# Performance work log

Measured on AMD Instinct MI355X. Metric: run time of the kernel, lower is better.

## Reference

```python
import jax, jax.numpy as jnp
import numpy as np
import math

D, H, FF, B, S = 512, 8, 2048, 2, 2048
DK = D // H


def _ln(x, g, b, eps=1e-5):
    m = jnp.mean(x, axis=-1, keepdims=True)
    v = jnp.var(x, axis=-1, keepdims=True)
    return (x - m) / jnp.sqrt(v + eps) * g + b


def _mha(q_in, kv_in, Wq, bq, Wk, bk, Wv, bv, Wo, bo):
    Bq, Sq, _ = q_in.shape
    Sk = kv_in.shape[1]
    q = (q_in @ Wq + bq).reshape(Bq, Sq, H, DK).transpose(0, 2, 1, 3)
    k = (kv_in @ Wk + bk).reshape(Bq, Sk, H, DK).transpose(0, 2, 1, 3)
    v = (kv_in @ Wv + bv).reshape(Bq, Sk, H, DK).transpose(0, 2, 1, 3)
    # NOTE: source uses float floor-division `//` by sqrt(dk); replicate faithfully.
    scores = jnp.floor(jnp.einsum('bhqd,bhkd->bhqk', q, k) / math.sqrt(DK))
    # NOTE: source calls scores.masked_fill(...) without assigning -> mask has no effect.
    attn = jax.nn.softmax(scores, axis=-1)
    out = jnp.einsum('bhqk,bhkd->bhqd', attn, v)
    out = out.transpose(0, 2, 1, 3).reshape(Bq, Sq, D)
    return out @ Wo + bo


def setup_inputs() -> dict:
    key = jax.random.key(0)
    ks = jax.random.split(key, 16)
    w = lambda k, shp: jax.random.normal(k, shp, jnp.float32) * 0.02
    inp = {
        'x': jax.random.normal(ks[0], (B, S, D), jnp.float32),
        'enc_out': jax.random.normal(ks[1], (B, S, D), jnp.float32),
        'src_mask': jnp.ones((B, 1, 1, S), jnp.int32),
        'tgt_mask': jnp.ones((B, 1, S, S), jnp.int32),
    }
    for i, pre in enumerate(['sa', 'ca']):
        kk = jax.random.split(ks[2 + i], 4)
        for j, nm in enumerate(['Wq', 'Wk', 'Wv', 'Wo']):
            inp[f'{pre}_{nm}'] = w(kk[j], (D, D))
            inp[f'{pre}_{nm[1].lower()}b'] = jnp.zeros((D,), jnp.float32)
    inp['ff_W1'] = w(ks[4], (D, FF)); inp['ff_b1'] = jnp.zeros((FF,), jnp.float32)
    inp['ff_W2'] = w(ks[5], (FF, D)); inp['ff_b2'] = jnp.zeros((D,), jnp.float32)
    for i in range(3):
        inp[f'ln{i}_g'] = jnp.ones((D,), jnp.float32)
        inp[f'ln{i}_b'] = jnp.zeros((D,), jnp.float32)
    return inp


def reference(x, enc_out, src_mask, tgt_mask,
              sa_Wq, sa_qb, sa_Wk, sa_kb, sa_Wv, sa_vb, sa_Wo, sa_ob,
              ca_Wq, ca_qb, ca_Wk, ca_kb, ca_Wv, ca_vb, ca_Wo, ca_ob,
              ff_W1, ff_b1, ff_W2, ff_b2,
              ln0_g, ln0_b, ln1_g, ln1_b, ln2_g, ln2_b):
    x = _ln(x + _mha(x, x, sa_Wq, sa_qb, sa_Wk, sa_kb, sa_Wv, sa_vb, sa_Wo, sa_ob), ln0_g, ln0_b)
    x = _ln(x + _mha(x, enc_out, ca_Wq, ca_qb, ca_Wk, ca_kb, ca_Wv, ca_vb, ca_Wo, ca_ob), ln1_g, ln1_b)
    ff = jax.nn.relu(x @ ff_W1 + ff_b1) @ ff_W2 + ff_b2
    x = _ln(x + ff, ln2_g, ln2_b)
    return x
```

## Files before the change

### kernel.cpp

```cpp
#include <hip/hip_runtime.h>
#include <math.h>


typedef __attribute__((ext_vector_type(8))) short short8;
typedef __attribute__((ext_vector_type(4))) float f32x4;

#define MFMA16(a, b, c) __builtin_amdgcn_mfma_f32_16x16x32_bf16((a), (b), (c), 0, 0, 0)

__device__ __forceinline__ unsigned short f2bf(float f) {
    unsigned int u = __float_as_uint(f);
    u += 0x7fffu + ((u >> 16) & 1u);
    return (unsigned short)(u >> 16);
}
__device__ __forceinline__ float bf2f(unsigned short h) {
    return __uint_as_float(((unsigned int)h) << 16);
}
__device__ __forceinline__ void g2l16(const void* g, void* l) {
    __builtin_amdgcn_global_load_lds(
        (const __attribute__((address_space(1))) unsigned int*)g,
        (__attribute__((address_space(3))) unsigned int*)l, 16, 0, 0);
}
__device__ __forceinline__ int swz(int row, int col) {
    return row * 64 + (col ^ ((row & 7) * 8));
}
__device__ __forceinline__ void xcd_remap(int& bx, int& by, int& bz) {
    const int gx = gridDim.x, gy = gridDim.y;
    const int nwg = gx * gy * gridDim.z;
    const int flat = blockIdx.x + gx * (blockIdx.y + gy * blockIdx.z);
    const int s = (flat & 7) * (nwg >> 3) + (flat >> 3);
    bx = s % gx; const int t = s / gx; by = t % gy; bz = t / gy;
}

template <int BM, int BN, int MODE>
__global__ __launch_bounds__(256, (BM == 64) ? 4 : (BN == 128 ? 2 : 3))
void gemm_bf16(
    const unsigned short* __restrict__ A, const unsigned short* __restrict__ Bt,
    const float* __restrict__ bias, float* __restrict__ Cf,
    unsigned short* __restrict__ O1,
    int M, int N, int K)
{
    __shared__ unsigned short As[2][BM * 64];
    __shared__ unsigned short Bs[2][BN * 64];
    const int tid = threadIdx.x, wv = tid >> 6, lane = tid & 63;
    const int l15 = lane & 15, l4 = lane >> 4;
    int bx, by, bz; xcd_remap(bx, by, bz);
    const int bm = by * BM, bn = bx * BN;
    constexpr int MI = (BM == 64) ? 1 : (BN == 128 ? 4 : 2);
    constexpr int AJ = (BM == 64) ? 2 : 4;
    constexpr int BJ = (BN == 128) ? 4 : 2;
    const int wrow = (BM == 64) ? wv * 16 : (BN == 128 ? (wv >> 1) * 64 : wv * 32);
    const int wcol = (BN == 128) ? (wv & 1) * 64 : 0;
    const int aw = (BM == 64) ? wv * 16 : wv * 32;
    const int bw = (BN == 128) ? wv * 32 : wv * 16;

    f32x4 acc[MI][4];
    #pragma unroll
    for (int i = 0; i < MI; ++i)
        #pragma unroll
        for (int j = 0; j < 4; ++j) acc[i][j] = (f32x4){0.f, 0.f, 0.f, 0.f};

    const int srow = lane >> 3;
    const int sch  = (lane & 7) ^ srow;
    const unsigned short* Asrc = A + (size_t)(bm + aw + srow) * K + sch * 8;
    const unsigned short* Bsrc = Bt + (size_t)(bn + bw + srow) * K + sch * 8;

    auto stage = [&](int buf, int k0) {
        #pragma unroll
        for (int j = 0; j < AJ; ++j)
            g2l16(Asrc + (size_t)j * 8 * K + k0, &As[buf][(aw + j * 8) * 64]);
        #pragma unroll
        for (int j = 0; j < BJ; ++j)
            g2l16(Bsrc + (size_t)j * 8 * K + k0, &Bs[buf][(bw + j * 8) * 64]);
    };

    stage(0, 0);
    __syncthreads();
    int cur = 0;
    for (int k0 = 0; k0 < K; k0 += 64) {
        if (k0 + 64 < K) stage(cur ^ 1, k0 + 64);
        #pragma unroll
        for (int kk = 0; kk < 2; ++kk) {
            const int kc = kk * 32 + l4 * 8;
            short8 af[MI], bfr[4];
            #pragma unroll
            for (int mi = 0; mi < MI; ++mi)
                af[mi] = *(const short8*)&As[cur][swz(wrow + mi * 16 + l15, kc)];
            #pragma unroll
            for (int nf = 0; nf < 4; ++nf)
                bfr[nf] = *(const short8*)&Bs[cur][swz(wcol + nf * 16 + l15, kc)];
            __builtin_amdgcn_s_setprio(1);
            #pragma unroll
            for (int mi = 0; mi < MI; ++mi)
                #pragma unroll
                for (int nf = 0; nf < 4; ++nf)
                    acc[mi][nf] = MFMA16(af[mi], bfr[nf], acc[mi][nf]);
            __builtin_amdgcn_s_setprio(0);
        }
        __syncthreads();
        cur ^= 1;
    }

    #pragma unroll
    for (int nf = 0; nf < 4; ++nf) {
        const int n = bn + wcol + nf * 16 + l15;
        const float bv = bias[n];
        #pragma unroll
        for (int mi = 0; mi < MI; ++mi) {
            const int m0 = bm + wrow + mi * 16 + l4 * 4;
            #pragma unroll
            for (int r = 0; r < 4; ++r) {
                float v = acc[mi][nf][r] + bv;
                size_t idx = (size_t)(m0 + r) * N + n;
                if (MODE == 0)      Cf[idx] = v;
                else if (MODE == 3) O1[idx] = f2bf(fmaxf(v, 0.f));
                else                O1[idx] = f2bf(v);
            }
        }
    }
}

struct QKVArgs {
    const unsigned short* A[3];
    const unsigned short* Bt[3];
    const float* bias[3];
    unsigned short* O1[3];
    int mode[3];
};
__global__ __launch_bounds__(256, 3) void qkv_gemm(QKVArgs ja)
{
    __shared__ unsigned short As[2][128 * 64];
    __shared__ unsigned short Bs[2][64 * 64];
    const int tid = threadIdx.x, wv = tid >> 6, lane = tid & 63;
    const int l15 = lane & 15, l4 = lane >> 4;
    int bx, by, bz; xcd_remap(bx, by, bz);
    const int bm = by * 128, bn = bx * 64;
    const unsigned short* A  = ja.A[bz];
    const unsigned short* Bt = ja.Bt[bz];
    const int mode = ja.mode[bz];

    f32x4 acc[2][4];
    #pragma unroll
    for (int i = 0; i < 2; ++i)
        #pragma unroll
        for (int j = 0; j < 4; ++j) acc[i][j] = (f32x4){0.f, 0.f, 0.f, 0.f};

    const int srow = lane >> 3, sch = (lane & 7) ^ srow;
    const unsigned short* Asrc = A + (size_t)(bm + wv * 32 + srow) * 512 + sch * 8;
    const unsigned short* Bsrc = Bt + (size_t)(bn + wv * 16 + srow) * 512 + sch * 8;

    auto stage = [&](int buf, int k0) {
        #pragma unroll
        for (int j = 0; j < 4; ++j)
            g2l16(Asrc + (size_t)j * 8 * 512 + k0, &As[buf][(wv * 32 + j * 8) * 64]);
        #pragma unroll
        for (int j = 0; j < 2; ++j)
            g2l16(Bsrc + (size_t)j * 8 * 512 + k0, &Bs[buf][(wv * 16 + j * 8) * 64]);
    };

    stage(0, 0);
    __syncthreads();
    int cur = 0;
    for (int k0 = 0; k0 < 512; k0 += 64) {
        if (k0 + 64 < 512) stage(cur ^ 1, k0 + 64);
        #pragma unroll
        for (int kk = 0; kk < 2; ++kk) {
            const int kc = kk * 32 + l4 * 8;
            short8 af[2], bfr[4];
            af[0] = *(const short8*)&As[cur][swz(wv * 32 + l15, kc)];
            af[1] = *(const short8*)&As[cur][swz(wv * 32 + 16 + l15, kc)];
            #pragma unroll
            for (int nf = 0; nf < 4; ++nf)
                bfr[nf] = *(const short8*)&Bs[cur][swz(nf * 16 + l15, kc)];
            __builtin_amdgcn_s_setprio(1);
            #pragma unroll
            for (int mi = 0; mi < 2; ++mi)
                #pragma unroll
                for (int nf = 0; nf < 4; ++nf)
                    acc[mi][nf] = MFMA16(af[mi], bfr[nf], acc[mi][nf]);
            __builtin_amdgcn_s_setprio(0);
        }
        __syncthreads();
        cur ^= 1;
    }

    #pragma unroll
    for (int nf = 0; nf < 4; ++nf) {
        const int n = bn + nf * 16 + l15;
        const float bv = ja.bias[bz][n];
        #pragma unroll
        for (int mi = 0; mi < 2; ++mi) {
            const int m0 = bm + wv * 32 + mi * 16 + l4 * 4;
            if (mode == 2) {
                const int hh = n >> 6, dd = n & 63, bb = m0 >> 11;
                const int key = m0 & 2047;
                const int f = (key & 63) >> 4, j0 = key & 15;
                const size_t basevt = (((size_t)bb * 8 + hh) * 64 + dd) * 2048
                                    + (key & ~63) + f;
                #pragma unroll
                for (int r = 0; r < 4; ++r)
                    ja.O1[bz][basevt + (size_t)(j0 + r) * 4] = f2bf(acc[mi][nf][r] + bv);
            } else {
                #pragma unroll
                for (int r = 0; r < 4; ++r)
                    ja.O1[bz][(size_t)(m0 + r) * 512 + n] = f2bf(acc[mi][nf][r] + bv);
            }
        }
    }
}

__global__ __launch_bounds__(256, 2) void attn_mfma(
    const unsigned short* __restrict__ Qb, const unsigned short* __restrict__ Kb,
    const unsigned short* __restrict__ Vt,
    float* __restrict__ PO0, float* __restrict__ PO1, float* __restrict__ PL)
{
    __shared__ unsigned short KH[2][64 * 64];
    __shared__ unsigned short VT[2][64 * 64];
    __shared__ unsigned short PS[64 * 64];

    const int tid = threadIdx.x, wv = tid >> 6, lane = tid & 63;
    const int l15 = lane & 15, l4 = lane >> 4;
    int bx, by, bz; xcd_remap(bx, by, bz);
    const int bh = by, b = bh >> 3, h = bh & 7;
    const int q0 = bx * 64;
    const int srow = lane >> 3;
    const int sch  = (lane & 7) ^ srow;
    const int kt0 = bz * 16, kt1 = kt0 + 16;

    short8 qh[2];
    {
        const size_t qrow = (size_t)(b * 2048 + q0 + wv * 16 + l15) * 512 + h * 64;
        qh[0] = *(const short8*)(Qb + qrow + l4 * 8);
        qh[1] = *(const short8*)(Qb + qrow + 32 + l4 * 8);
    }

    const unsigned short* k_src  = Kb + (size_t)(b * 2048 + wv * 16 + srow) * 512 + h * 64 + sch * 8;
    const unsigned short* vt_src = Vt + (size_t)(bh * 64 + wv * 16 + srow) * 2048 + sch * 8;

    auto stageKV = [&](int buf, int kt) {
        const size_t k0 = (size_t)kt * 64;
        #pragma unroll
        for (int j = 0; j < 2; ++j) {
            g2l16(k_src + (k0 + j * 8) * 512, &KH[buf][(wv * 16 + j * 8) * 64]);
            g2l16(vt_src + k0 + (size_t)j * 8 * 2048, &VT[buf][(wv * 16 + j * 8) * 64]);
        }
    };

    f32x4 o[4], lacc;
    #pragma unroll
    for (int i = 0; i < 4; ++i) o[i] = (f32x4){0.f, 0.f, 0.f, 0.f};
    lacc = (f32x4){0.f, 0.f, 0.f, 0.f};

    const short one_s = (short)(l15 == 0 ? 0x3F80 : 0);
    const short8 oneb = {one_s, one_s, one_s, one_s, one_s, one_s, one_s, one_s};

    stageKV(0, kt0);
    __syncthreads();
    int cur = 0;
    for (int kt = kt0; kt < kt1; ++kt) {
        if (kt + 1 < kt1) stageKV(cur ^ 1, kt + 1);

        f32x4 s[4];
        __builtin_amdgcn_s_setprio(1);
        #pragma unroll
        for (int f = 0; f < 4; ++f) {
            s[f] = (f32x4){0.f, 0.f, 0.f, 0.f};
            #pragma unroll
            for (int kk = 0; kk < 2; ++kk) {
                short8 kbf = *(const short8*)&KH[cur][swz(f * 16 + l15, kk * 32 + l4 * 8)];
                s[f] = MFMA16(qh[kk], kbf, s[f]);
            }
        }
        __builtin_amdgcn_s_setprio(0);

        #pragma unroll
        for (int r = 0; r < 4; ++r) {
            float p0 = __expf(floorf(s[0][r] * 0.125f));
            float p1 = __expf(floorf(s[1][r] * 0.125f));
            float p2 = __expf(floorf(s[2][r] * 0.125f));
            float p3 = __expf(floorf(s[3][r] * 0.125f));
            unsigned u0, u1;
            asm("v_cvt_pk_bf16_f32 %0, %1, %2" : "=v"(u0) : "v"(p0), "v"(p1));
            asm("v_cvt_pk_bf16_f32 %0, %1, %2" : "=v"(u1) : "v"(p2), "v"(p3));
            *(uint2*)&PS[swz(wv * 16 + l4 * 4 + r, l15 * 4)] = (uint2){u0, u1};
        }

        short8 pa[2];
        pa[0] = *(const short8*)&PS[swz(wv * 16 + l15, l4 * 8)];
        pa[1] = *(const short8*)&PS[swz(wv * 16 + l15, 32 + l4 * 8)];

        __builtin_amdgcn_s_setprio(1);
        lacc = MFMA16(pa[0], oneb, lacc);
        lacc = MFMA16(pa[1], oneb, lacc);
        #pragma unroll
        for (int df = 0; df < 4; ++df) {
            #pragma unroll
            for (int kk = 0; kk < 2; ++kk) {
                short8 vb = *(const short8*)&VT[cur][swz(df * 16 + l15, kk * 32 + l4 * 8)];
                o[df] = MFMA16(pa[kk], vb, o[df]);
            }
        }
        __builtin_amdgcn_s_setprio(0);
        __syncthreads();
        cur ^= 1;
    }

    float* PO = bz ? PO1 : PO0;
    #pragma unroll
    for (int df = 0; df < 4; ++df)
        #pragma unroll
        for (int r = 0; r < 4; ++r)
            PO[(size_t)(b * 2048 + q0 + wv * 16 + l4 * 4 + r) * 512 + h * 64 + df * 16 + l15]
                = o[df][r];
    if (l15 == 0) {
        #pragma unroll
        for (int r = 0; r < 4; ++r)
            PL[(bz * 16 + bh) * 2048 + q0 + wv * 16 + l4 * 4 + r] = lacc[r];
    }
}

__global__ __launch_bounds__(256) void attn_combine(
    const float* __restrict__ po0, const float* __restrict__ po1,
    const float* __restrict__ pl, unsigned short* __restrict__ Ob)
{
    const size_t i = ((size_t)blockIdx.x * 256 + threadIdx.x) * 8;
    const int row = (int)(i >> 9), col = (int)(i & 511);
    const int b = row >> 11, q = row & 2047, h = col >> 6;
    const int bh = b * 8 + h;
    const float inv = 1.f / (pl[bh * 2048 + q] + pl[(16 + bh) * 2048 + q]);
    float4 a0 = *(const float4*)(po0 + i), a1 = *(const float4*)(po0 + i + 4);
    float4 c0 = *(const float4*)(po1 + i), c1 = *(const float4*)(po1 + i + 4);
    uint4 u;
    u.x = (unsigned)f2bf((a0.x + c0.x) * inv) | ((unsigned)f2bf((a0.y + c0.y) * inv) << 16);
    u.y = (unsigned)f2bf((a0.z + c0.z) * inv) | ((unsigned)f2bf((a0.w + c0.w) * inv) << 16);
    u.z = (unsigned)f2bf((a1.x + c1.x) * inv) | ((unsigned)f2bf((a1.y + c1.y) * inv) << 16);
    u.w = (unsigned)f2bf((a1.z + c1.z) * inv) | ((unsigned)f2bf((a1.w + c1.w) * inv) << 16);
    *(uint4*)(Ob + i) = u;
}

template <bool XBF, bool RBF, bool OUTF, bool OUTB>
__global__ __launch_bounds__(256) void add_ln(
    const void* __restrict__ Xv, const void* __restrict__ Rv,
    const float* __restrict__ g, const float* __restrict__ beta,
    float* __restrict__ OutF, unsigned short* __restrict__ OutB)
{
    const int row = blockIdx.x * 4 + (threadIdx.x >> 6);
    const int lane = threadIdx.x & 63;
    const int c0 = lane * 8;
    float xx[8], rr[8], v[8];
    if (XBF) {
        const unsigned short* xr = (const unsigned short*)Xv + (size_t)row * 512 + c0;
        uint4 u = *(const uint4*)xr;
        xx[0] = bf2f(u.x & 0xffff); xx[1] = bf2f(u.x >> 16);
        xx[2] = bf2f(u.y & 0xffff); xx[3] = bf2f(u.y >> 16);
        xx[4] = bf2f(u.z & 0xffff); xx[5] = bf2f(u.z >> 16);
        xx[6] = bf2f(u.w & 0xffff); xx[7] = bf2f(u.w >> 16);
    } else {
        const float* xr = (const float*)Xv + (size_t)row * 512 + c0;
        float4 a0 = *(const float4*)xr, a1 = *(const float4*)(xr + 4);
        xx[0] = a0.x; xx[1] = a0.y; xx[2] = a0.z; xx[3] = a0.w;
        xx[4] = a1.x; xx[5] = a1.y; xx[6] = a1.z; xx[7] = a1.w;
    }
    if (RBF) {
        const unsigned short* xr = (const unsigned short*)Rv + (size_t)row * 512 + c0;
        uint4 u = *(const uint4*)xr;
        rr[0] = bf2f(u.x & 0xffff); rr[1] = bf2f(u.x >> 16);
        rr[2] = bf2f(u.y & 0xffff); rr[3] = bf2f(u.y >> 16);
        rr[4] = bf2f(u.z & 0xffff); rr[5] = bf2f(u.z >> 16);
        rr[6] = bf2f(u.w & 0xffff); rr[7] = bf2f(u.w >> 16);
    } else {
        const float* xr = (const float*)Rv + (size_t)row * 512 + c0;
        float4 a0 = *(const float4*)xr, a1 = *(const float4*)(xr + 4);
        rr[0] = a0.x; rr[1] = a0.y; rr[2] = a0.z; rr[3] = a0.w;
        rr[4] = a1.x; rr[5] = a1.y; rr[6] = a1.z; rr[7] = a1.w;
    }
    float s = 0.f, s2 = 0.f;
    #pragma unroll
    for (int j = 0; j < 8; ++j) {
        v[j] = xx[j] + rr[j];
        s += v[j]; s2 += v[j] * v[j];
    }
    #pragma unroll
    for (int off = 1; off < 64; off <<= 1) {
        s  += __shfl_xor(s, off);
        s2 += __shfl_xor(s2, off);
    }
    const float mean = s * (1.f / 512.f);
    const float var = s2 * (1.f / 512.f) - mean * mean;
    const float rs = 1.f / sqrtf(var + 1e-5f);
    float ovals[8];
    const float* gg = g + c0; const float* bb = beta + c0;
    #pragma unroll
    for (int j = 0; j < 8; ++j) ovals[j] = (v[j] - mean) * rs * gg[j] + bb[j];
    if (OUTF) {
        float* po = OutF + (size_t)row * 512 + c0;
        *(float4*)po = (float4){ovals[0], ovals[1], ovals[2], ovals[3]};
        *(float4*)(po + 4) = (float4){ovals[4], ovals[5], ovals[6], ovals[7]};
    }
    if (OUTB) {
        uint4 u;
        u.x = (unsigned)f2bf(ovals[0]) | ((unsigned)f2bf(ovals[1]) << 16);
        u.y = (unsigned)f2bf(ovals[2]) | ((unsigned)f2bf(ovals[3]) << 16);
        u.z = (unsigned)f2bf(ovals[4]) | ((unsigned)f2bf(ovals[5]) << 16);
        u.w = (unsigned)f2bf(ovals[6]) | ((unsigned)f2bf(ovals[7]) << 16);
        *(uint4*)(OutB + (size_t)row * 512 + c0) = u;
    }
}

struct WTJobs {
    const float* src[10];
    unsigned short* dst[10];
    int K[10], N[10];
    int cum[11];
};
__global__ __launch_bounds__(256) void prep(
    const float* __restrict__ X, const float* __restrict__ E,
    unsigned short* __restrict__ Xb, unsigned short* __restrict__ Eb, WTJobs jb)
{
    __shared__ float T[32][33];
    const int bid = blockIdx.x;
    if (bid < 2048) {
        size_t i = ((size_t)bid * 256 + threadIdx.x) * 8;
        const float* src; unsigned short* dst; size_t off;
        if (i < 2097152) { src = X; dst = Xb; off = i; }
        else             { src = E; dst = Eb; off = i - 2097152; }
        float4 a = *(const float4*)(src + off), c = *(const float4*)(src + off + 4);
        uint4 u;
        u.x = (unsigned)f2bf(a.x) | ((unsigned)f2bf(a.y) << 16);
        u.y = (unsigned)f2bf(a.z) | ((unsigned)f2bf(a.w) << 16);
        u.z = (unsigned)f2bf(c.x) | ((unsigned)f2bf(c.y) << 16);
        u.w = (unsigned)f2bf(c.z) | ((unsigned)f2bf(c.w) << 16);
        *(uint4*)(dst + off) = u;
        return;
    }
    int wb = bid - 2048;
    int z = 0;
    while (wb >= jb.cum[z + 1]) ++z;
    const int lt = wb - jb.cum[z];
    const int K = jb.K[z], N = jb.N[z];
    const int ntx = N >> 5;
    const int tx = lt % ntx, ty = lt / ntx;
    const int r = threadIdx.x >> 3, c4 = (threadIdx.x & 7) * 4;
    float4 a = *(const float4*)(jb.src[z] + (size_t)(ty * 32 + r) * N + tx * 32 + c4);
    T[r][c4] = a.x; T[r][c4 + 1] = a.y; T[r][c4 + 2] = a.z; T[r][c4 + 3] = a.w;
    __syncthreads();
    ushort4 o;
    o.x = f2bf(T[c4][r]); o.y = f2bf(T[c4 + 1][r]);
    o.z = f2bf(T[c4 + 2][r]); o.w = f2bf(T[c4 + 3][r]);
    *(ushort4*)(jb.dst[z] + (size_t)(tx * 32 + r) * K + ty * 32 + c4) = o;
}

extern "C" void kernel_launch(void* const* d_in, const int* in_sizes, int n_in,
                              void* d_out, int out_size, void* d_ws, size_t ws_size,
                              hipStream_t stream)
{
    const float* x   = (const float*)d_in[0];
    const float* enc = (const float*)d_in[1];
    const float* Wp[8] = {(const float*)d_in[4],  (const float*)d_in[6],
                          (const float*)d_in[8],  (const float*)d_in[10],
                          (const float*)d_in[12], (const float*)d_in[14],
                          (const float*)d_in[16], (const float*)d_in[18]};
    const float* sa_qb = (const float*)d_in[5],  *sa_kb = (const float*)d_in[7];
    const float* sa_vb = (const float*)d_in[9],  *sa_ob = (const float*)d_in[11];
    const float* ca_qb = (const float*)d_in[13], *ca_kb = (const float*)d_in[15];
    const float* ca_vb = (const float*)d_in[17], *ca_ob = (const float*)d_in[19];
    const float* ff_W1 = (const float*)d_in[20], *ff_b1 = (const float*)d_in[21];
    const float* ff_W2 = (const float*)d_in[22], *ff_b2 = (const float*)d_in[23];
    const float* ln0_g = (const float*)d_in[24], *ln0_b = (const float*)d_in[25];
    const float* ln1_g = (const float*)d_in[26], *ln1_b = (const float*)d_in[27];
    const float* ln2_g = (const float*)d_in[28], *ln2_b = (const float*)d_in[29];

    char* base = (char*)d_ws;
    const size_t MB = 1u << 20;
    unsigned short* wt    = (unsigned short*)(base + 0 * MB);
    unsigned short* xb    = (unsigned short*)(base + 8 * MB);
    unsigned short* encb  = (unsigned short*)(base + 12 * MB);
    unsigned short* x1b   = (unsigned short*)(base + 16 * MB);
    unsigned short* attnb = (unsigned short*)(base + 20 * MB);
    unsigned short* vt    = (unsigned short*)(base + 24 * MB);
    unsigned short* qb    = (unsigned short*)(base + 28 * MB);
    unsigned short* kb    = (unsigned short*)(base + 32 * MB);
    float*          pl    = (float*)(base + 36 * MB);
    unsigned short* projb = (unsigned short*)(base + 44 * MB);
    float*          po0   = (float*)(base + 48 * MB);
    unsigned short* ffb   = qb;
    unsigned short* x2b   = xb;
    float* po1 = (float*)d_out;
    float* out = (float*)d_out;

    unsigned short* wtp[10];
    for (int i = 0; i < 8; ++i) wtp[i] = wt + (size_t)i * 262144;
    wtp[8] = wt + 8u * 262144;
    wtp[9] = wt + 8u * 262144 + 1048576;

    WTJobs jb;
    for (int i = 0; i < 8; ++i) { jb.src[i] = Wp[i]; jb.dst[i] = wtp[i]; jb.K[i] = 512; jb.N[i] = 512; }
    jb.src[8] = ff_W1; jb.dst[8] = wtp[8]; jb.K[8] = 512;  jb.N[8] = 2048;
    jb.src[9] = ff_W2; jb.dst[9] = wtp[9]; jb.K[9] = 2048; jb.N[9] = 512;
    jb.cum[0] = 0;
    for (int i = 0; i < 10; ++i)
        jb.cum[i + 1] = jb.cum[i] + (jb.N[i] >> 5) * (jb.K[i] >> 5);

    QKVArgs sa, ca;
    sa.A[0] = xb;  sa.Bt[0] = wtp[0]; sa.bias[0] = sa_qb; sa.O1[0] = qb; sa.mode[0] = 4;
    sa.A[1] = xb;  sa.Bt[1] = wtp[1]; sa.bias[1] = sa_kb; sa.O1[1] = kb; sa.mode[1] = 4;
    sa.A[2] = xb;  sa.Bt[2] = wtp[2]; sa.bias[2] = sa_vb; sa.O1[2] = vt; sa.mode[2] = 2;
    ca.A[0] = x1b;  ca.Bt[0] = wtp[4]; ca.bias[0] = ca_qb; ca.O1[0] = qb; ca.mode[0] = 4;
    ca.A[1] = encb; ca.Bt[1] = wtp[5]; ca.bias[1] = ca_kb; ca.O1[1] = kb; ca.mode[1] = 4;
    ca.A[2] = encb; ca.Bt[2] = wtp[6]; ca.bias[2] = ca_vb; ca.O1[2] = vt; ca.mode[2] = 2;

    dim3 blk(256);
    dim3 gqkv(8, 32, 3);
    dim3 g64(8, 64);
    dim3 gff1(16, 32);
    dim3 gattn(32, 16, 2);
    dim3 gln(1024);

    prep<<<2048 + jb.cum[10], blk, 0, stream>>>(x, enc, xb, encb, jb);

    qkv_gemm<<<gqkv, blk, 0, stream>>>(sa);
    attn_mfma<<<gattn, blk, 0, stream>>>(qb, kb, vt, po0, po1, pl);
    attn_combine<<<1024, blk, 0, stream>>>(po0, po1, pl, attnb);
    gemm_bf16<64, 64, 4><<<g64, blk, 0, stream>>>(attnb, wtp[3], sa_ob, nullptr, projb, 4096, 512, 512);
    add_ln<false, true, false, true><<<gln, blk, 0, stream>>>(x, projb, ln0_g, ln0_b, nullptr, x1b);

    qkv_gemm<<<gqkv, blk, 0, stream>>>(ca);
    attn_mfma<<<gattn, blk, 0, stream>>>(qb, kb, vt, po0, po1, pl);
    attn_combine<<<1024, blk, 0, stream>>>(po0, po1, pl, attnb);
    gemm_bf16<64, 64, 4><<<g64, blk, 0, stream>>>(attnb, wtp[7], ca_ob, nullptr, projb, 4096, 512, 512);
    add_ln<true, true, false, true><<<gln, blk, 0, stream>>>(x1b, projb, ln1_g, ln1_b, nullptr, x2b);

    gemm_bf16<128, 128, 3><<<gff1, blk, 0, stream>>>(x2b, wtp[8], ff_b1, nullptr, ffb, 4096, 2048, 512);
    gemm_bf16<64, 64, 4><<<g64, blk, 0, stream>>>(ffb, wtp[9], ff_b2, nullptr, projb, 4096, 512, 2048);
    add_ln<true, true, true, false><<<gln, blk, 0, stream>>>(x2b, projb, ln2_g, ln2_b, out, nullptr);
}
```

Before: 193.0 us.

## Store attention partials in bf16 and use natural-order V transpose layout

The split-K attention kernel now writes its two partial outputs as bf16 instead of fp32, and the combine kernel reads them back as bf16. This halves the partial-output traffic and moves the second buffer off the output tensor. The V-transpose epilogue now writes keys in natural order with one vectorized 4-element store instead of four scattered stores. The softmax P tile is written to LDS as individual truncated bf16 values in the matching natural column order. This trades some precision (bf16 partials, truncation instead of rounding) and more, narrower LDS stores for less global memory traffic.

```diff
diff --git a/kernel.cpp b/kernel.cpp
--- a/kernel.cpp
+++ b/kernel.cpp
@@ -191,14 +191,13 @@
         for (int mi = 0; mi < 2; ++mi) {
             const int m0 = bm + wv * 32 + mi * 16 + l4 * 4;
             if (mode == 2) {
-                const int hh = n >> 6, dd = n & 63, bb = m0 >> 11;
-                const int key = m0 & 2047;
-                const int f = (key & 63) >> 4, j0 = key & 15;
-                const size_t basevt = (((size_t)bb * 8 + hh) * 64 + dd) * 2048
-                                    + (key & ~63) + f;
-                #pragma unroll
-                for (int r = 0; r < 4; ++r)
-                    ja.O1[bz][basevt + (size_t)(j0 + r) * 4] = f2bf(acc[mi][nf][r] + bv);
+                ushort4 pk;
+                pk.x = f2bf(acc[mi][nf][0] + bv);
+                pk.y = f2bf(acc[mi][nf][1] + bv);
+                pk.z = f2bf(acc[mi][nf][2] + bv);
+                pk.w = f2bf(acc[mi][nf][3] + bv);
+                const int hh = n >> 6, dd = n & 63, bb = m0 >> 11, key = m0 & 2047;
+                *(ushort4*)(ja.O1[bz] + ((((size_t)bb * 8 + hh) * 64 + dd) * 2048 + key)) = pk;
             } else {
                 #pragma unroll
                 for (int r = 0; r < 4; ++r)
@@ -211,7 +210,8 @@
 __global__ __launch_bounds__(256, 2) void attn_mfma(
     const unsigned short* __restrict__ Qb, const unsigned short* __restrict__ Kb,
     const unsigned short* __restrict__ Vt,
-    float* __restrict__ PO0, float* __restrict__ PO1, float* __restrict__ PL)
+    unsigned short* __restrict__ PO0, unsigned short* __restrict__ PO1,
+    float* __restrict__ PL)
 {
     __shared__ unsigned short KH[2][64 * 64];
     __shared__ unsigned short VT[2][64 * 64];
@@ -273,16 +273,11 @@
         __builtin_amdgcn_s_setprio(0);
 
         #pragma unroll
-        for (int r = 0; r < 4; ++r) {
-            float p0 = __expf(floorf(s[0][r] * 0.125f));
-            float p1 = __expf(floorf(s[1][r] * 0.125f));
-            float p2 = __expf(floorf(s[2][r] * 0.125f));
-            float p3 = __expf(floorf(s[3][r] * 0.125f));
-            unsigned u0, u1;
-            asm("v_cvt_pk_bf16_f32 %0, %1, %2" : "=v"(u0) : "v"(p0), "v"(p1));
-            asm("v_cvt_pk_bf16_f32 %0, %1, %2" : "=v"(u1) : "v"(p2), "v"(p3));
-            *(uint2*)&PS[swz(wv * 16 + l4 * 4 + r, l15 * 4)] = (uint2){u0, u1};
-        }
+        for (int f = 0; f < 4; ++f)
+            #pragma unroll
+            for (int r = 0; r < 4; ++r)
+                PS[swz(wv * 16 + l4 * 4 + r, f * 16 + l15)] =
+                    (unsigned short)(__float_as_uint(__expf(floorf(s[f][r] * 0.125f))) >> 16);
 
         short8 pa[2];
         pa[0] = *(const short8*)&PS[swz(wv * 16 + l15, l4 * 8)];
@@ -304,13 +299,13 @@
         cur ^= 1;
     }
 
-    float* PO = bz ? PO1 : PO0;
+    unsigned short* PO = bz ? PO1 : PO0;
     #pragma unroll
     for (int df = 0; df < 4; ++df)
         #pragma unroll
         for (int r = 0; r < 4; ++r)
             PO[(size_t)(b * 2048 + q0 + wv * 16 + l4 * 4 + r) * 512 + h * 64 + df * 16 + l15]
-                = o[df][r];
+                = f2bf(o[df][r]);
     if (l15 == 0) {
         #pragma unroll
         for (int r = 0; r < 4; ++r)
@@ -319,7 +314,7 @@
 }
 
 __global__ __launch_bounds__(256) void attn_combine(
-    const float* __restrict__ po0, const float* __restrict__ po1,
+    const unsigned short* __restrict__ po0, const unsigned short* __restrict__ po1,
     const float* __restrict__ pl, unsigned short* __restrict__ Ob)
 {
     const size_t i = ((size_t)blockIdx.x * 256 + threadIdx.x) * 8;
@@ -327,13 +322,16 @@
     const int b = row >> 11, q = row & 2047, h = col >> 6;
     const int bh = b * 8 + h;
     const float inv = 1.f / (pl[bh * 2048 + q] + pl[(16 + bh) * 2048 + q]);
-    float4 a0 = *(const float4*)(po0 + i), a1 = *(const float4*)(po0 + i + 4);
-    float4 c0 = *(const float4*)(po1 + i), c1 = *(const float4*)(po1 + i + 4);
+    uint4 a = *(const uint4*)(po0 + i);
+    uint4 c = *(const uint4*)(po1 + i);
     uint4 u;
-    u.x = (unsigned)f2bf((a0.x + c0.x) * inv) | ((unsigned)f2bf((a0.y + c0.y) * inv) << 16);
-    u.y = (unsigned)f2bf((a0.z + c0.z) * inv) | ((unsigned)f2bf((a0.w + c0.w) * inv) << 16);
-    u.z = (unsigned)f2bf((a1.x + c1.x) * inv) | ((unsigned)f2bf((a1.y + c1.y) * inv) << 16);
-    u.w = (unsigned)f2bf((a1.z + c1.z) * inv) | ((unsigned)f2bf((a1.w + c1.w) * inv) << 16);
+    unsigned* ap = (unsigned*)&a; unsigned* cp = (unsigned*)&c; unsigned* up = (unsigned*)&u;
+    #pragma unroll
+    for (int w = 0; w < 4; ++w) {
+        float lo = (bf2f(ap[w] & 0xffff) + bf2f(cp[w] & 0xffff)) * inv;
+        float hi = (bf2f(ap[w] >> 16)   + bf2f(cp[w] >> 16))   * inv;
+        up[w] = (unsigned)f2bf(lo) | ((unsigned)f2bf(hi) << 16);
+    }
     *(uint4*)(Ob + i) = u;
 }
 
@@ -481,10 +479,10 @@
     unsigned short* kb    = (unsigned short*)(base + 32 * MB);
     float*          pl    = (float*)(base + 36 * MB);
     unsigned short* projb = (unsigned short*)(base + 44 * MB);
-    float*          po0   = (float*)(base + 48 * MB);
+    unsigned short* po0   = (unsigned short*)(base + 48 * MB);
+    unsigned short* po1   = (unsigned short*)(base + 52 * MB);
     unsigned short* ffb   = qb;
     unsigned short* x2b   = xb;
-    float* po1 = (float*)d_out;
     float* out = (float*)d_out;
 
     unsigned short* wtp[10];
```

After: 171.8 us. 11.0% less time.
